# Performance work log

Hardware: AMD Instinct MI355X
Metric: run time of the kernel (lower is better)

The kernel has to match this reference:

```python
import jax, jax.numpy as jnp
import numpy as np

BINS = 10
MOMENTUM = 0.5


def setup_inputs() -> dict:
    key = jax.random.key(0)
    k1, k2 = jax.random.split(key)
    B, D = 4096, 512
    x = jax.random.normal(k1, (B, D), dtype=jnp.float32)
    targets = jax.random.randint(k2, (B,), 0, 100, dtype=jnp.int64)
    acc_sum = jnp.zeros((BINS,), dtype=jnp.float32)
    return {"x": x, "acc_sum": acc_sum, "targets": targets}


def reference(x, acc_sum, targets):
    bins, momentum = BINS, MOMENTUM
    B = x.shape[0]
    # bin edges: arange(bins+1)/bins, last edge bumped by 1e-6
    edges = jnp.arange(bins + 1, dtype=jnp.float32) / bins
    edges = edges.at[-1].add(1e-6)

    # F.normalize: x / max(||x||_2, 1e-12) row-wise
    norm = jnp.maximum(jnp.linalg.norm(x, axis=1, keepdims=True), 1e-12)
    xn = x / norm
    cos = xn @ xn.T  # [B, B]

    label = (targets[:, None] == targets[None, :]).astype(jnp.float32)  # [B, B]

    g = jnp.abs(cos - label).ravel()  # gradient-density statistic, in [0, 2]
    # bin index i such that edges[i] <= g < edges[i+1]
    idx = jnp.searchsorted(edges, g, side="right") - 1
    valid = (idx >= 0) & (idx < bins)  # g >= edges[-1] falls in no bin -> weight 0

    # fused histogram (replaces the 10-iteration mask loop)
    counts = jnp.bincount(jnp.where(valid, idx, bins), length=bins + 1)[:bins]
    counts = counts.astype(jnp.float32)

    tot = jnp.float32(B * B)
    acc_new = momentum * acc_sum + (1.0 - momentum) * counts  # EMA update (momentum > 0 path)
    w_bin = tot / (acc_new + 1e-6)  # per-bin weight

    weights = jnp.where(valid, w_bin[jnp.clip(idx, 0, bins - 1)], 0.0)
    valid_num = jnp.sum(counts)
    weights = jnp.where(valid_num > 0, weights / valid_num, weights)

    loss = jnp.mean((label.ravel() - cos.ravel()) ** 2 * weights)
    return loss
```

## Files before the change

kernel.cpp:

```cpp
#include <hip/hip_runtime.h>
#include <hip/hip_bf16.h>

typedef __bf16 bf16x8 __attribute__((ext_vector_type(8)));
typedef float f32x4 __attribute__((ext_vector_type(4)));

typedef __attribute__((address_space(1))) void GAS;
typedef __attribute__((address_space(3))) void LAS;
#define GLOAD16(gp, lp) __builtin_amdgcn_global_load_lds((GAS*)(gp), (LAS*)(lp), 16, 0, 0)

#define NB 4096
#define NDU 1024
#define NKT 16
#define NBLK 256

__global__ __launch_bounds__(256) void nrm_split_k(const float* __restrict__ x,
                                                   __bf16* __restrict__ u,
                                                   float* __restrict__ part,
                                                   int* __restrict__ ticket) {
    if (blockIdx.x < 20) part[blockIdx.x * NBLK + threadIdx.x] = 0.0f;
    if (blockIdx.x == 20 && threadIdx.x == 0) *ticket = 0;
    const int wid = threadIdx.x >> 6, lane = threadIdx.x & 63;
    const int row = blockIdx.x * 4 + wid;
    const float4* xr = reinterpret_cast<const float4*>(x + (size_t)row * 512);
    float4 v0 = xr[lane * 2 + 0];
    float4 v1 = xr[lane * 2 + 1];
    float xv[8] = {v0.x, v0.y, v0.z, v0.w, v1.x, v1.y, v1.z, v1.w};
    float ss = 0.0f;
#pragma unroll
    for (int j = 0; j < 8; ++j) ss += xv[j] * xv[j];
#pragma unroll
    for (int off = 32; off > 0; off >>= 1) ss += __shfl_xor(ss, off);
    const float rn = 1.0f / fmaxf(sqrtf(ss), 1e-12f);
    bf16x8 h, l;
#pragma unroll
    for (int j = 0; j < 8; ++j) {
        float xn = xv[j] * rn;
        __bf16 hb = (__bf16)xn;
        h[j] = hb;
        l[j] = (__bf16)(xn - (float)hb);
    }
    reinterpret_cast<bf16x8*>(u + (size_t)row * NDU)[lane] = h;
    reinterpret_cast<bf16x8*>(u + (size_t)row * NDU + 512)[lane] = l;
}

__global__ __launch_bounds__(512, 2) void gemm_stat_k(const __bf16* __restrict__ u,
                                                      const int* __restrict__ targets,
                                                      const float* __restrict__ acc_sum,
                                                      float* __restrict__ part,
                                                      int* __restrict__ ticket,
                                                      float* __restrict__ out) {
    __shared__ __align__(16) __bf16 lds[2][2][2][128 * 64];
    __shared__ int tgtR[256], tgtC[256];
    __shared__ float red_s[8][10], red_c[8][10];
    __shared__ float tot[20];
    __shared__ int is_last;

    const int bid = blockIdx.x;
    const int swz = (bid & 7) * 32 + (bid >> 3);
    const int by = swz >> 4, bx = swz & 15;
    const int row0 = by * 256, col0 = bx * 256;
    const int tid = threadIdx.x, lane = tid & 63;
    const int wid = tid >> 6, wr = wid >> 2, wc = wid & 3;

    if (tid < 256) tgtR[tid] = targets[row0 + tid];
    else           tgtC[tid - 256] = targets[col0 + tid - 256];

    const int c0 = tid, c1 = tid + 512;
    const int r0c = c0 >> 3, x0 = ((c0 & 7) ^ (r0c & 7)) * 8;
    const int r1c = c1 >> 3, x1 = ((c1 & 7) ^ (r1c & 7)) * 8;

    auto STAGE = [&](int s) {
        const int kt = s >> 2, h4 = s & 3;
        const int slot = kt & 1, kcol = kt * 64;
        const bool isA = (h4 < 2);
        const int half = h4 & 1;
        const int brow = (isA ? row0 : col0) + half * 128;
        __bf16* ldst = &lds[slot][isA ? 0 : 1][half][0];
        GLOAD16(u + (size_t)(brow + r0c) * NDU + kcol + x0, ldst + c0 * 8);
        GLOAD16(u + (size_t)(brow + r1c) * NDU + kcol + x1, ldst + c1 * 8);
    };

    const f32x4 fzero = {0.0f, 0.0f, 0.0f, 0.0f};
    f32x4 acc[8][4];
#pragma unroll
    for (int a = 0; a < 8; ++a)
#pragma unroll
        for (int n = 0; n < 4; ++n) acc[a][n] = fzero;

    STAGE(0); STAGE(1); STAGE(2); STAGE(3); STAGE(4);
    asm volatile("s_waitcnt vmcnt(2)" ::: "memory");
    __builtin_amdgcn_s_barrier();
    __builtin_amdgcn_sched_barrier(0);

    const int fr = lane & 15, hi16 = lane >> 4;
    const int Bhalf = wc >> 1;

    for (int kt = 0; kt < NKT; ++kt) {
        const int slot = kt & 1;
        const __bf16* lA = &lds[slot][0][0][0];
        const __bf16* lB = &lds[slot][1][Bhalf][0];
#pragma unroll
        for (int f = 0; f < 4; ++f) {
            const int Mh = f >> 1, kh = f & 1;
            bf16x8 af[4], bf[4];
#pragma unroll
            for (int q = 0; q < 4; ++q) {
                const int row = wr * 64 + q * 16 + fr;
                const int cb = (kh * 64 + hi16 * 16) ^ ((row & 7) << 4);
                af[q] = *(const bf16x8*)((const char*)(lA + Mh * 8192) + row * 128 + cb);
            }
#pragma unroll
            for (int n = 0; n < 4; ++n) {
                const int row = (wc & 1) * 64 + n * 16 + fr;
                const int cb = (kh * 64 + hi16 * 16) ^ ((row & 7) << 4);
                bf[n] = *(const bf16x8*)((const char*)lB + row * 128 + cb);
            }
            const int s = 4 * kt + f + 5;
            if (s < 4 * NKT) STAGE(s);
            __builtin_amdgcn_s_barrier();
            __builtin_amdgcn_sched_barrier(0);
            __builtin_amdgcn_s_setprio(1);
#pragma unroll
            for (int q = 0; q < 4; ++q)
#pragma unroll
                for (int n = 0; n < 4; ++n)
                    acc[Mh * 4 + q][n] = __builtin_amdgcn_mfma_f32_16x16x32_bf16(
                        af[q], bf[n], acc[Mh * 4 + q][n], 0, 0, 0);
            __builtin_amdgcn_s_setprio(0);
            __builtin_amdgcn_sched_barrier(0);
            if (f == 3) {
                if (kt < NKT - 2)       asm volatile("s_waitcnt vmcnt(2)" ::: "memory");
                else if (kt == NKT - 2) asm volatile("s_waitcnt vmcnt(0)" ::: "memory");
            }
            __builtin_amdgcn_s_barrier();
            __builtin_amdgcn_sched_barrier(0);
        }
    }

    int tcv[4];
#pragma unroll
    for (int n = 0; n < 4; ++n) tcv[n] = tgtC[wc * 64 + n * 16 + fr];

    constexpr float E[11] = {0.0f, 0.1f, 0.2f, 0.3f, 0.4f, 0.5f,
                             0.6f, 0.7f, 0.8f, 0.9f, 1.0f + 1e-6f};
    float sacc[10], cacc[10];
#pragma unroll
    for (int b = 0; b < 10; ++b) { sacc[b] = 0.0f; cacc[b] = 0.0f; }

    const int rB = wr * 64 + hi16 * 4;
#pragma unroll
    for (int a = 0; a < 8; ++a) {
        int trv[4];
#pragma unroll
        for (int r = 0; r < 4; ++r) trv[r] = tgtR[(a >> 2) * 128 + rB + (a & 3) * 16 + r];
#pragma unroll
        for (int n = 0; n < 4; ++n) {
            f32x4 v = acc[a][n];
            const int tc = tcv[n];
#pragma unroll
            for (int r = 0; r < 4; ++r) {
                const float label = (trv[r] == tc) ? 1.0f : 0.0f;
                const float g = fabsf(v[r] - label);
                const float g2 = g * g;
                bool prev = true;
#pragma unroll
                for (int b = 0; b < 10; ++b) {
                    const bool ge = (g >= E[b + 1]);
                    const bool in = prev && (!ge);
                    sacc[b] += in ? g2 : 0.0f;
                    cacc[b] += in ? 1.0f : 0.0f;
                    prev = ge;
                }
            }
        }
    }

#pragma unroll
    for (int b = 0; b < 10; ++b) {
        float sv = sacc[b], cv = cacc[b];
#pragma unroll
        for (int off = 32; off > 0; off >>= 1) {
            sv += __shfl_xor(sv, off);
            cv += __shfl_xor(cv, off);
        }
        if (lane == 0) { red_s[wid][b] = sv; red_c[wid][b] = cv; }
    }
    __syncthreads();

    if (tid < 10) {
        float s = 0.0f, c = 0.0f;
#pragma unroll
        for (int w = 0; w < 8; ++w) { s += red_s[w][tid]; c += red_c[w][tid]; }
        __hip_atomic_store(&part[tid * NBLK + bid], s,
                           __ATOMIC_RELAXED, __HIP_MEMORY_SCOPE_AGENT);
        __hip_atomic_store(&part[(10 + tid) * NBLK + bid], c,
                           __ATOMIC_RELAXED, __HIP_MEMORY_SCOPE_AGENT);
    }
    __syncthreads();

    if (tid == 0) {
        int old = __hip_atomic_fetch_add(ticket, 1, __ATOMIC_ACQ_REL,
                                         __HIP_MEMORY_SCOPE_AGENT);
        is_last = (old == NBLK - 1) ? 1 : 0;
    }
    __syncthreads();

    if (is_last) {
        for (int b = wid; b < 20; b += 8) {
            float v = 0.0f;
#pragma unroll
            for (int j = 0; j < 4; ++j)
                v += __hip_atomic_load(&part[b * NBLK + lane + 64 * j],
                                       __ATOMIC_RELAXED, __HIP_MEMORY_SCOPE_AGENT);
#pragma unroll
            for (int off = 32; off > 0; off >>= 1) v += __shfl_xor(v, off);
            if (lane == 0) tot[b] = v;
        }
        __syncthreads();
        if (tid == 0) {
            const float totN = 16777216.0f;
            double num = 0.0, valid = 0.0;
#pragma unroll
            for (int b = 0; b < 10; ++b) {
                float cnt = tot[10 + b];
                float accn = 0.5f * acc_sum[b] + 0.5f * cnt;
                float w = totN / (accn + 1e-6f);
                num += (double)tot[b] * (double)w;
                valid += (double)cnt;
            }
            out[0] = (valid > 0.0) ? (float)(num / valid / 16777216.0) : 0.0f;
        }
    }
}

extern "C" void kernel_launch(void* const* d_in, const int* in_sizes, int n_in,
                              void* d_out, int out_size, void* d_ws, size_t ws_size,
                              hipStream_t stream) {
    const float* x = (const float*)d_in[0];
    const float* acc_sum = (const float*)d_in[1];
    const int* targets = (const int*)d_in[2];
    float* out = (float*)d_out;

    char* ws = (char*)d_ws;
    __bf16* u = (__bf16*)ws;
    float* part = (float*)(ws + (size_t)NB * NDU * sizeof(__bf16));
    int* ticket = (int*)(part + 20 * NBLK);

    nrm_split_k<<<NB / 4, 256, 0, stream>>>(x, u, part, ticket);
    gemm_stat_k<<<NBLK, 512, 0, stream>>>(u, targets, acc_sum, part, ticket, out);
}
```

Baseline: 157.9 us.

## Exploit Gram symmetry: compute upper-triangular 128x128 tiles with doubled off-diagonal weight

Result: slower. 177.3 us (+12.3%).

```diff
diff --git a/kernel.cpp b/kernel.cpp
--- a/kernel.cpp
+++ b/kernel.cpp
@@ -10,14 +10,19 @@
 
 #define NB 4096
 #define NDU 1024
-#define NKT 16
-#define NBLK 256
+#define BK 32
+#define NSTEP 32
+#define NTI 32
+#define NBLK2 528
+#define PSTR 576
 
 __global__ __launch_bounds__(256) void nrm_split_k(const float* __restrict__ x,
                                                    __bf16* __restrict__ u,
                                                    float* __restrict__ part,
                                                    int* __restrict__ ticket) {
-    if (blockIdx.x < 20) part[blockIdx.x * NBLK + threadIdx.x] = 0.0f;
+    if (blockIdx.x < 20) {
+        for (int i = threadIdx.x; i < PSTR; i += 256) part[blockIdx.x * PSTR + i] = 0.0f;
+    }
     if (blockIdx.x == 20 && threadIdx.x == 0) *ticket = 0;
     const int wid = threadIdx.x >> 6, lane = threadIdx.x & 63;
     const int row = blockIdx.x * 4 + wid;
@@ -43,98 +48,85 @@
     reinterpret_cast<bf16x8*>(u + (size_t)row * NDU + 512)[lane] = l;
 }
 
-__global__ __launch_bounds__(512, 2) void gemm_stat_k(const __bf16* __restrict__ u,
-                                                      const int* __restrict__ targets,
-                                                      const float* __restrict__ acc_sum,
-                                                      float* __restrict__ part,
-                                                      int* __restrict__ ticket,
-                                                      float* __restrict__ out) {
-    __shared__ __align__(16) __bf16 lds[2][2][2][128 * 64];
-    __shared__ int tgtR[256], tgtC[256];
-    __shared__ float red_s[8][10], red_c[8][10];
+__global__ __launch_bounds__(256) void gemm_stat_k(const __bf16* __restrict__ u,
+                                                   const int* __restrict__ targets,
+                                                   const float* __restrict__ acc_sum,
+                                                   float* __restrict__ part,
+                                                   int* __restrict__ ticket,
+                                                   float* __restrict__ out) {
+    __shared__ __align__(16) __bf16 lds[2][2][128 * BK];
+    __shared__ int tgtR[128], tgtC[128];
+    __shared__ float red_s[4][10], red_c[4][10];
     __shared__ float tot[20];
     __shared__ int is_last;
 
-    const int bid = blockIdx.x;
-    const int swz = (bid & 7) * 32 + (bid >> 3);
-    const int by = swz >> 4, bx = swz & 15;
-    const int row0 = by * 256, col0 = bx * 256;
+    const int s = (blockIdx.x & 7) * 66 + (blockIdx.x >> 3);
+    int by = (int)((65.0f - sqrtf((float)(4225 - 8 * s))) * 0.5f);
+    int base = 32 * by - ((by * (by - 1)) >> 1);
+    if (s < base) { --by; base = 32 * by - ((by * (by - 1)) >> 1); }
+    else if (s >= base + (NTI - by)) { ++by; base = 32 * by - ((by * (by - 1)) >> 1); }
+    const int bx = by + (s - base);
+    const int row0 = by * 128, col0 = bx * 128;
+    const float wgt = (by == bx) ? 1.0f : 2.0f;
+
     const int tid = threadIdx.x, lane = tid & 63;
-    const int wid = tid >> 6, wr = wid >> 2, wc = wid & 3;
-
-    if (tid < 256) tgtR[tid] = targets[row0 + tid];
-    else           tgtC[tid - 256] = targets[col0 + tid - 256];
-
-    const int c0 = tid, c1 = tid + 512;
-    const int r0c = c0 >> 3, x0 = ((c0 & 7) ^ (r0c & 7)) * 8;
-    const int r1c = c1 >> 3, x1 = ((c1 & 7) ^ (r1c & 7)) * 8;
-
-    auto STAGE = [&](int s) {
-        const int kt = s >> 2, h4 = s & 3;
-        const int slot = kt & 1, kcol = kt * 64;
-        const bool isA = (h4 < 2);
-        const int half = h4 & 1;
-        const int brow = (isA ? row0 : col0) + half * 128;
-        __bf16* ldst = &lds[slot][isA ? 0 : 1][half][0];
-        GLOAD16(u + (size_t)(brow + r0c) * NDU + kcol + x0, ldst + c0 * 8);
-        GLOAD16(u + (size_t)(brow + r1c) * NDU + kcol + x1, ldst + c1 * 8);
+    const int wid = tid >> 6, wr = wid >> 1, wc = wid & 1;
+
+    if (tid < 128) tgtR[tid] = targets[row0 + tid];
+    else           tgtC[tid - 128] = targets[col0 + tid - 128];
+
+    const int r0 = tid >> 2,          c0 = tid & 3;
+    const int r1 = (tid + 256) >> 2,  c1 = tid & 3;
+    const int sc0 = (c0 ^ ((r0 >> 1) & 3)) * 8;
+    const int sc1 = (c1 ^ ((r1 >> 1) & 3)) * 8;
+    const __bf16* Aq0 = u + (size_t)(row0 + r0) * NDU + sc0;
+    const __bf16* Aq1 = u + (size_t)(row0 + r1) * NDU + sc1;
+    const __bf16* Bq0 = u + (size_t)(col0 + r0) * NDU + sc0;
+    const __bf16* Bq1 = u + (size_t)(col0 + r1) * NDU + sc1;
+    const int d0 = tid * 8, d1 = (tid + 256) * 8;
+
+    auto STAGE = [&](int t) {
+        const int buf = t & 1, kc = t * BK;
+        GLOAD16(Aq0 + kc, &lds[buf][0][d0]);
+        GLOAD16(Aq1 + kc, &lds[buf][0][d1]);
+        GLOAD16(Bq0 + kc, &lds[buf][1][d0]);
+        GLOAD16(Bq1 + kc, &lds[buf][1][d1]);
     };
 
+    const int fr = lane & 15, hi16 = lane >> 4;
+    const int kb_sw = ((hi16 ^ ((fr >> 1) & 3))) * 8;
+    int rowA[4], rowB[4];
+#pragma unroll
+    for (int m = 0; m < 4; ++m) rowA[m] = (wr * 64 + m * 16 + fr) * BK + kb_sw;
+#pragma unroll
+    for (int n = 0; n < 4; ++n) rowB[n] = (wc * 64 + n * 16 + fr) * BK + kb_sw;
+
     const f32x4 fzero = {0.0f, 0.0f, 0.0f, 0.0f};
-    f32x4 acc[8][4];
-#pragma unroll
-    for (int a = 0; a < 8; ++a)
-#pragma unroll
-        for (int n = 0; n < 4; ++n) acc[a][n] = fzero;
-
-    STAGE(0); STAGE(1); STAGE(2); STAGE(3); STAGE(4);
-    asm volatile("s_waitcnt vmcnt(2)" ::: "memory");
-    __builtin_amdgcn_s_barrier();
-    __builtin_amdgcn_sched_barrier(0);
-
-    const int fr = lane & 15, hi16 = lane >> 4;
-    const int Bhalf = wc >> 1;
-
-    for (int kt = 0; kt < NKT; ++kt) {
-        const int slot = kt & 1;
-        const __bf16* lA = &lds[slot][0][0][0];
-        const __bf16* lB = &lds[slot][1][Bhalf][0];
-#pragma unroll
-        for (int f = 0; f < 4; ++f) {
-            const int Mh = f >> 1, kh = f & 1;
-            bf16x8 af[4], bf[4];
-#pragma unroll
-            for (int q = 0; q < 4; ++q) {
-                const int row = wr * 64 + q * 16 + fr;
-                const int cb = (kh * 64 + hi16 * 16) ^ ((row & 7) << 4);
-                af[q] = *(const bf16x8*)((const char*)(lA + Mh * 8192) + row * 128 + cb);
-            }
-#pragma unroll
-            for (int n = 0; n < 4; ++n) {
-                const int row = (wc & 1) * 64 + n * 16 + fr;
-                const int cb = (kh * 64 + hi16 * 16) ^ ((row & 7) << 4);
-                bf[n] = *(const bf16x8*)((const char*)lB + row * 128 + cb);
-            }
-            const int s = 4 * kt + f + 5;
-            if (s < 4 * NKT) STAGE(s);
-            __builtin_amdgcn_s_barrier();
-            __builtin_amdgcn_sched_barrier(0);
-            __builtin_amdgcn_s_setprio(1);
-#pragma unroll
-            for (int q = 0; q < 4; ++q)
-#pragma unroll
-                for (int n = 0; n < 4; ++n)
-                    acc[Mh * 4 + q][n] = __builtin_amdgcn_mfma_f32_16x16x32_bf16(
-                        af[q], bf[n], acc[Mh * 4 + q][n], 0, 0, 0);
-            __builtin_amdgcn_s_setprio(0);
-            __builtin_amdgcn_sched_barrier(0);
-            if (f == 3) {
-                if (kt < NKT - 2)       asm volatile("s_waitcnt vmcnt(2)" ::: "memory");
-                else if (kt == NKT - 2) asm volatile("s_waitcnt vmcnt(0)" ::: "memory");
-            }
-            __builtin_amdgcn_s_barrier();
-            __builtin_amdgcn_sched_barrier(0);
-        }
+    f32x4 acc[4][4];
+#pragma unroll
+    for (int m = 0; m < 4; ++m)
+#pragma unroll
+        for (int n = 0; n < 4; ++n) acc[m][n] = fzero;
+
+    STAGE(0);
+    __syncthreads();
+
+    for (int t = 0; t < NSTEP; ++t) {
+        if (t + 1 < NSTEP) STAGE(t + 1);
+        const int buf = t & 1;
+        const __bf16* lA = &lds[buf][0][0];
+        const __bf16* lB = &lds[buf][1][0];
+        bf16x8 af[4], bf[4];
+#pragma unroll
+        for (int m = 0; m < 4; ++m) af[m] = *reinterpret_cast<const bf16x8*>(lA + rowA[m]);
+#pragma unroll
+        for (int n = 0; n < 4; ++n) bf[n] = *reinterpret_cast<const bf16x8*>(lB + rowB[n]);
+#pragma unroll
+        for (int m = 0; m < 4; ++m)
+#pragma unroll
+            for (int n = 0; n < 4; ++n)
+                acc[m][n] = __builtin_amdgcn_mfma_f32_16x16x32_bf16(af[m], bf[n], acc[m][n], 0, 0, 0);
+        __syncthreads();
     }
 
     int tcv[4];
@@ -149,13 +141,13 @@
 
     const int rB = wr * 64 + hi16 * 4;
 #pragma unroll
-    for (int a = 0; a < 8; ++a) {
+    for (int m = 0; m < 4; ++m) {
         int trv[4];
 #pragma unroll
-        for (int r = 0; r < 4; ++r) trv[r] = tgtR[(a >> 2) * 128 + rB + (a & 3) * 16 + r];
+        for (int r = 0; r < 4; ++r) trv[r] = tgtR[rB + m * 16 + r];
 #pragma unroll
         for (int n = 0; n < 4; ++n) {
-            f32x4 v = acc[a][n];
+            f32x4 v = acc[m][n];
             const int tc = tcv[n];
 #pragma unroll
             for (int r = 0; r < 4; ++r) {
@@ -183,17 +175,17 @@
             sv += __shfl_xor(sv, off);
             cv += __shfl_xor(cv, off);
         }
-        if (lane == 0) { red_s[wid][b] = sv; red_c[wid][b] = cv; }
+        if (lane == 0) { red_s[wid][b] = sv * wgt; red_c[wid][b] = cv * wgt; }
     }
     __syncthreads();
 
     if (tid < 10) {
-        float s = 0.0f, c = 0.0f;
-#pragma unroll
-        for (int w = 0; w < 8; ++w) { s += red_s[w][tid]; c += red_c[w][tid]; }
-        __hip_atomic_store(&part[tid * NBLK + bid], s,
+        float sv = 0.0f, cv = 0.0f;
+#pragma unroll
+        for (int w = 0; w < 4; ++w) { sv += red_s[w][tid]; cv += red_c[w][tid]; }
+        __hip_atomic_store(&part[tid * PSTR + s], sv,
                            __ATOMIC_RELAXED, __HIP_MEMORY_SCOPE_AGENT);
-        __hip_atomic_store(&part[(10 + tid) * NBLK + bid], c,
+        __hip_atomic_store(&part[(10 + tid) * PSTR + s], cv,
                            __ATOMIC_RELAXED, __HIP_MEMORY_SCOPE_AGENT);
     }
     __syncthreads();
@@ -201,16 +193,16 @@
     if (tid == 0) {
         int old = __hip_atomic_fetch_add(ticket, 1, __ATOMIC_ACQ_REL,
                                          __HIP_MEMORY_SCOPE_AGENT);
-        is_last = (old == NBLK - 1) ? 1 : 0;
+        is_last = (old == NBLK2 - 1) ? 1 : 0;
     }
     __syncthreads();
 
     if (is_last) {
-        for (int b = wid; b < 20; b += 8) {
+        for (int b = wid; b < 20; b += 4) {
             float v = 0.0f;
 #pragma unroll
-            for (int j = 0; j < 4; ++j)
-                v += __hip_atomic_load(&part[b * NBLK + lane + 64 * j],
+            for (int j = 0; j < 9; ++j)
+                v += __hip_atomic_load(&part[b * PSTR + lane + 64 * j],
                                        __ATOMIC_RELAXED, __HIP_MEMORY_SCOPE_AGENT);
 #pragma unroll
             for (int off = 32; off > 0; off >>= 1) v += __shfl_xor(v, off);
@@ -244,8 +236,8 @@
     char* ws = (char*)d_ws;
     __bf16* u = (__bf16*)ws;
     float* part = (float*)(ws + (size_t)NB * NDU * sizeof(__bf16));
-    int* ticket = (int*)(part + 20 * NBLK);
+    int* ticket = (int*)(part + 20 * PSTR);
 
     nrm_split_k<<<NB / 4, 256, 0, stream>>>(x, u, part, ticket);
-    gemm_stat_k<<<NBLK, 512, 0, stream>>>(u, targets, acc_sum, part, ticket, out);
+    gemm_stat_k<<<NBLK2, 256, 0, stream>>>(u, targets, acc_sum, part, ticket, out);
 }
```
